# Kernel optimization log

Hardware: AMD Instinct MI355X
Metric: run time of the kernel (lower is better)

## Reference

```python
import jax, jax.numpy as jnp
import numpy as np

B, C = 8192, 10000
POS_RATE = 0.005  # ~50 positives per row on average


def setup_inputs() -> dict:
    key = jax.random.key(0)
    k1, k2, k3 = jax.random.split(key, 3)
    output = jax.random.normal(k1, (B, C), dtype=jnp.float32)
    # sparse binary multilabels, guaranteed >=1 positive per row
    ml = (jax.random.uniform(k2, (B, C)) < POS_RATE).astype(jnp.float32)
    gt = jax.random.randint(k3, (B,), 0, C)  # guaranteed ground-truth label per row
    ml = ml.at[jnp.arange(B), gt].set(1.0)
    return {"output": output, "multilabels": ml}


def reference(output, multilabels):
    # Original torch code log_softmaxes `output`, then feeds the result to
    # F.cross_entropy which applies log_softmax AGAIN -> double log_softmax.
    o = jax.nn.log_softmax(output, axis=1)
    o2 = jax.nn.log_softmax(o, axis=1)
    # per-sample loss = min over targets t of -o2[i, t] = -max over targets of o2[i, t]
    neg_inf = jnp.float32(-jnp.inf)
    masked = jnp.where(multilabels == 1.0, o2, neg_inf)
    per_sample = -jnp.max(masked, axis=1)
    return jnp.mean(per_sample)
```

## Files before the change

kernel.cpp:

```cpp
#include <hip/hip_runtime.h>
#include <math.h>

#define NROWS 8192
#define NCOLS 10000
#define NVEC  (NCOLS / 4)
#define ROWS_PER_BLOCK 4
#define NBLOCKS (NROWS / ROWS_PER_BLOCK)

typedef float vfloat4 __attribute__((ext_vector_type(4)));

__global__ __launch_bounds__(256) void min_ce_kernel(
    const float* __restrict__ output,
    const float* __restrict__ ml,
    float* __restrict__ ws)
{
    const int wave = threadIdx.x >> 6;
    const int lane = threadIdx.x & 63;
    const int row  = blockIdx.x * ROWS_PER_BLOCK + wave;

    const vfloat4* __restrict__ orow = (const vfloat4*)(output + (size_t)row * NCOLS);
    const vfloat4* __restrict__ mrow = (const vfloat4*)(ml     + (size_t)row * NCOLS);

    const float L2E = 1.4426950408889634f;
    float s0 = 0.f, s1 = 0.f, s2 = 0.f, s3 = 0.f;
    float m0 = -INFINITY, m1 = -INFINITY, m2 = -INFINITY, m3 = -INFINITY;

    #pragma unroll 8
    for (int i = lane; i < NVEC; i += 64) {
        vfloat4 x = __builtin_nontemporal_load(&orow[i]);
        vfloat4 t = __builtin_nontemporal_load(&mrow[i]);

        s0 += __builtin_amdgcn_exp2f(__builtin_fmaf(x.x, L2E, -8.0f));
        s1 += __builtin_amdgcn_exp2f(__builtin_fmaf(x.y, L2E, -8.0f));
        s2 += __builtin_amdgcn_exp2f(__builtin_fmaf(x.z, L2E, -8.0f));
        s3 += __builtin_amdgcn_exp2f(__builtin_fmaf(x.w, L2E, -8.0f));

        m0 = fmaxf(m0, t.x == 1.0f ? x.x : -INFINITY);
        m1 = fmaxf(m1, t.y == 1.0f ? x.y : -INFINITY);
        m2 = fmaxf(m2, t.z == 1.0f ? x.z : -INFINITY);
        m3 = fmaxf(m3, t.w == 1.0f ? x.w : -INFINITY);
    }

    float s  = (s0 + s1) + (s2 + s3);
    float mp = fmaxf(fmaxf(m0, m1), fmaxf(m2, m3));

    #pragma unroll
    for (int off = 32; off >= 1; off >>= 1) {
        s += __shfl_xor(s, off);
        mp = fmaxf(mp, __shfl_xor(mp, off));
    }

    if (lane == 0) {
        float loss = 0.69314718055994531f * (__log2f(s) + 8.0f) - mp;
        ws[row] = loss * (1.0f / (float)NROWS);
    }
}

__global__ __launch_bounds__(256) void final_reduce_kernel(
    const float* __restrict__ ws, float* __restrict__ out)
{
    const vfloat4* __restrict__ w4 = (const vfloat4*)ws;
    float v = 0.f;
    #pragma unroll
    for (int i = threadIdx.x; i < NROWS / 4; i += 256) {
        vfloat4 x = w4[i];
        v += (x.x + x.y) + (x.z + x.w);
    }
    #pragma unroll
    for (int off = 32; off >= 1; off >>= 1) v += __shfl_xor(v, off);

    __shared__ float sv[4];
    const int wave = threadIdx.x >> 6;
    const int lane = threadIdx.x & 63;
    if (lane == 0) sv[wave] = v;
    __syncthreads();
    if (threadIdx.x == 0) out[0] = (sv[0] + sv[1]) + (sv[2] + sv[3]);
}

extern "C" void kernel_launch(void* const* d_in, const int* in_sizes, int n_in,
                              void* d_out, int out_size, void* d_ws, size_t ws_size,
                              hipStream_t stream) {
    const float* output = (const float*)d_in[0];
    const float* ml     = (const float*)d_in[1];
    float* out = (float*)d_out;
    float* ws  = (float*)d_ws;

    min_ce_kernel<<<NBLOCKS, 256, 0, stream>>>(output, ml, ws);
    final_reduce_kernel<<<1, 256, 0, stream>>>(ws, out);
}
```

Measured before the change: 584.7 us.

## Split rows into 64-vector windows with atomic per-row sum and max accumulation

Each wave now handles a 256-float window of a row instead of a whole row. Windows are spread grid-stride across a fixed number of waves, and each window's partial exp-sum and masked max go into per-row workspace through float atomicAdd and an order-preserving unsigned atomicMax. An init kernel clears the workspace first, and the final kernel does the log and the subtraction per row. The aim is finer-grained load balancing, at the cost of atomic traffic, an extra launch, one load per lane per iteration with no unrolling, and a float atomic sum order that is no longer deterministic.

```diff
diff --git a/kernel.cpp b/kernel.cpp
--- a/kernel.cpp
+++ b/kernel.cpp
@@ -4,67 +4,85 @@
 #define NROWS 8192
 #define NCOLS 10000
 #define NVEC  (NCOLS / 4)
-#define ROWS_PER_BLOCK 4
-#define NBLOCKS (NROWS / ROWS_PER_BLOCK)
+#define WIN_PER_ROW 40
+#define NWAVES 8192
+#define NWIN (NROWS * WIN_PER_ROW)
 
 typedef float vfloat4 __attribute__((ext_vector_type(4)));
+
+__device__ __forceinline__ unsigned fkey(float f) {
+    int u = __float_as_int(f);
+    return (unsigned)(u ^ ((u >> 31) | 0x80000000));
+}
+__device__ __forceinline__ float fdecode(unsigned k) {
+    int u = (k & 0x80000000u) ? (int)(k ^ 0x80000000u) : (int)(~k);
+    return __int_as_float(u);
+}
+
+__global__ __launch_bounds__(256) void init_ws_kernel(float* wsum, unsigned* wmax) {
+    const int i = blockIdx.x * 256 + threadIdx.x;
+    wsum[i] = 0.0f;
+    wmax[i] = 0x007FFFFFu;
+}
 
 __global__ __launch_bounds__(256) void min_ce_kernel(
     const float* __restrict__ output,
     const float* __restrict__ ml,
-    float* __restrict__ ws)
+    float* __restrict__ wsum,
+    unsigned* __restrict__ wmax)
 {
     const int wave = threadIdx.x >> 6;
     const int lane = threadIdx.x & 63;
-    const int row  = blockIdx.x * ROWS_PER_BLOCK + wave;
+    const int W = blockIdx.x * 4 + wave;
+    const float L2E = 1.4426950408889634f;
 
-    const vfloat4* __restrict__ orow = (const vfloat4*)(output + (size_t)row * NCOLS);
-    const vfloat4* __restrict__ mrow = (const vfloat4*)(ml     + (size_t)row * NCOLS);
+    for (int w = W; w < NWIN; w += NWAVES) {
+        const int row = w / WIN_PER_ROW;
+        const int win = w - row * WIN_PER_ROW;
+        const int v4  = win * 64 + lane;
 
-    const float L2E = 1.4426950408889634f;
-    float s0 = 0.f, s1 = 0.f, s2 = 0.f, s3 = 0.f;
-    float m0 = -INFINITY, m1 = -INFINITY, m2 = -INFINITY, m3 = -INFINITY;
+        float s  = 0.0f;
+        float mp = -INFINITY;
+        if (v4 < NVEC) {
+            const vfloat4* __restrict__ o4 = (const vfloat4*)(output + (size_t)row * NCOLS);
+            const vfloat4* __restrict__ m4 = (const vfloat4*)(ml     + (size_t)row * NCOLS);
+            vfloat4 x = __builtin_nontemporal_load(&o4[v4]);
+            vfloat4 t = __builtin_nontemporal_load(&m4[v4]);
 
-    #pragma unroll 8
-    for (int i = lane; i < NVEC; i += 64) {
-        vfloat4 x = __builtin_nontemporal_load(&orow[i]);
-        vfloat4 t = __builtin_nontemporal_load(&mrow[i]);
+            float e0 = __builtin_amdgcn_exp2f(__builtin_fmaf(x.x, L2E, -8.0f));
+            float e1 = __builtin_amdgcn_exp2f(__builtin_fmaf(x.y, L2E, -8.0f));
+            float e2 = __builtin_amdgcn_exp2f(__builtin_fmaf(x.z, L2E, -8.0f));
+            float e3 = __builtin_amdgcn_exp2f(__builtin_fmaf(x.w, L2E, -8.0f));
+            s = (e0 + e1) + (e2 + e3);
 
-        s0 += __builtin_amdgcn_exp2f(__builtin_fmaf(x.x, L2E, -8.0f));
-        s1 += __builtin_amdgcn_exp2f(__builtin_fmaf(x.y, L2E, -8.0f));
-        s2 += __builtin_amdgcn_exp2f(__builtin_fmaf(x.z, L2E, -8.0f));
-        s3 += __builtin_amdgcn_exp2f(__builtin_fmaf(x.w, L2E, -8.0f));
+            float a = fmaxf(t.x == 1.0f ? x.x : -INFINITY,
+                            t.y == 1.0f ? x.y : -INFINITY);
+            float b = fmaxf(t.z == 1.0f ? x.z : -INFINITY,
+                            t.w == 1.0f ? x.w : -INFINITY);
+            mp = fmaxf(a, b);
+        }
 
-        m0 = fmaxf(m0, t.x == 1.0f ? x.x : -INFINITY);
-        m1 = fmaxf(m1, t.y == 1.0f ? x.y : -INFINITY);
-        m2 = fmaxf(m2, t.z == 1.0f ? x.z : -INFINITY);
-        m3 = fmaxf(m3, t.w == 1.0f ? x.w : -INFINITY);
-    }
+        #pragma unroll
+        for (int off = 32; off >= 1; off >>= 1) {
+            s += __shfl_xor(s, off);
+            mp = fmaxf(mp, __shfl_xor(mp, off));
+        }
 
-    float s  = (s0 + s1) + (s2 + s3);
-    float mp = fmaxf(fmaxf(m0, m1), fmaxf(m2, m3));
-
-    #pragma unroll
-    for (int off = 32; off >= 1; off >>= 1) {
-        s += __shfl_xor(s, off);
-        mp = fmaxf(mp, __shfl_xor(mp, off));
-    }
-
-    if (lane == 0) {
-        float loss = 0.69314718055994531f * (__log2f(s) + 8.0f) - mp;
-        ws[row] = loss * (1.0f / (float)NROWS);
+        if (lane == 0) {
+            atomicAdd(&wsum[row], s);
+            if (mp > -INFINITY) atomicMax(&wmax[row], fkey(mp));
+        }
     }
 }
 
 __global__ __launch_bounds__(256) void final_reduce_kernel(
-    const float* __restrict__ ws, float* __restrict__ out)
+    const float* __restrict__ wsum, const unsigned* __restrict__ wmax,
+    float* __restrict__ out)
 {
-    const vfloat4* __restrict__ w4 = (const vfloat4*)ws;
-    float v = 0.f;
-    #pragma unroll
-    for (int i = threadIdx.x; i < NROWS / 4; i += 256) {
-        vfloat4 x = w4[i];
-        v += (x.x + x.y) + (x.z + x.w);
+    float v = 0.0f;
+    for (int i = threadIdx.x; i < NROWS; i += 256) {
+        float loss = 0.69314718055994531f * (__log2f(wsum[i]) + 8.0f) - fdecode(wmax[i]);
+        v += loss;
     }
     #pragma unroll
     for (int off = 32; off >= 1; off >>= 1) v += __shfl_xor(v, off);
@@ -74,7 +92,7 @@
     const int lane = threadIdx.x & 63;
     if (lane == 0) sv[wave] = v;
     __syncthreads();
-    if (threadIdx.x == 0) out[0] = (sv[0] + sv[1]) + (sv[2] + sv[3]);
+    if (threadIdx.x == 0) out[0] = ((sv[0] + sv[1]) + (sv[2] + sv[3])) * (1.0f / (float)NROWS);
 }
 
 extern "C" void kernel_launch(void* const* d_in, const int* in_sizes, int n_in,
@@ -83,8 +101,10 @@
     const float* output = (const float*)d_in[0];
     const float* ml     = (const float*)d_in[1];
     float* out = (float*)d_out;
-    float* ws  = (float*)d_ws;
+    float* wsum = (float*)d_ws;
+    unsigned* wmax = (unsigned*)d_ws + NROWS;
 
-    min_ce_kernel<<<NBLOCKS, 256, 0, stream>>>(output, ml, ws);
-    final_reduce_kernel<<<1, 256, 0, stream>>>(ws, out);
+    init_ws_kernel<<<NROWS / 256, 256, 0, stream>>>(wsum, wmax);
+    min_ce_kernel<<<NWAVES / 4, 256, 0, stream>>>(output, ml, wsum, wmax);
+    final_reduce_kernel<<<1, 256, 0, stream>>>(wsum, wmax, out);
 }
```

Result: slower. 629.6 us (+7.7%).
